# Performance work log

Hardware: AMD Instinct MI355X
Metric: run time of the kernel (lower is better)

The kernel has to match this reference:

```python
import jax, jax.numpy as jnp
import numpy as np

D = 64          # slot_size == in_features
S = 8           # num_slots
H = 128         # mlp_hidden_size
N_ITER = 3
EPS = 1e-8


def _ln(x, g, b, eps=1e-5):
    m = jnp.mean(x, axis=-1, keepdims=True)
    v = jnp.var(x, axis=-1, keepdims=True)
    return (x - m) * jax.lax.rsqrt(v + eps) * g + b


def _gru(x, h, w_ih, w_hh, b_ih, b_hh):
    # torch.nn.GRUCell semantics, gate order r, z, n
    gi = x @ w_ih.T + b_ih
    gh = h @ w_hh.T + b_hh
    i_r, i_z, i_n = jnp.split(gi, 3, axis=-1)
    h_r, h_z, h_n = jnp.split(gh, 3, axis=-1)
    r = jax.nn.sigmoid(i_r + h_r)
    z = jax.nn.sigmoid(i_z + h_z)
    n = jnp.tanh(i_n + r * h_n)
    return (1.0 - z) * n + z * h


def setup_inputs() -> dict:
    key = jax.random.key(0)
    ks = jax.random.split(key, 16)
    sc = 0.02
    inp = {
        'inputs': jax.random.normal(ks[0], (64, 16384, D), jnp.float32),
        'slots_init': jax.random.normal(ks[1], (64, S, D), jnp.float32),
        'ln_in_g': jnp.ones((D,), jnp.float32), 'ln_in_b': jnp.zeros((D,), jnp.float32),
        'ln_s_g': jnp.ones((D,), jnp.float32), 'ln_s_b': jnp.zeros((D,), jnp.float32),
        'ln_m_g': jnp.ones((D,), jnp.float32), 'ln_m_b': jnp.zeros((D,), jnp.float32),
        'Wq': jax.random.normal(ks[2], (D, D), jnp.float32) * sc,
        'Wk': jax.random.normal(ks[3], (D, D), jnp.float32) * sc,
        'Wv': jax.random.normal(ks[4], (D, D), jnp.float32) * sc,
        'w_ih': jax.random.normal(ks[5], (3 * D, D), jnp.float32) * sc,
        'w_hh': jax.random.normal(ks[6], (3 * D, D), jnp.float32) * sc,
        'b_ih': jnp.zeros((3 * D,), jnp.float32),
        'b_hh': jnp.zeros((3 * D,), jnp.float32),
        'W1': jax.random.normal(ks[7], (H, D), jnp.float32) * sc,
        'b1': jnp.zeros((H,), jnp.float32),
        'W2': jax.random.normal(ks[8], (D, H), jnp.float32) * sc,
        'b2': jnp.zeros((D,), jnp.float32),
        'slots_mu': jax.random.normal(ks[9], (1, 1, D), jnp.float32) * sc,
        'slots_log_sigma': jax.random.normal(ks[10], (1, 1, D), jnp.float32) * sc,
    }
    return inp


def reference(inputs, slots_init, ln_in_g, ln_in_b, ln_s_g, ln_s_b, ln_m_g, ln_m_b,
              Wq, Wk, Wv, w_ih, w_hh, b_ih, b_hh, W1, b1, W2, b2,
              slots_mu, slots_log_sigma):
    B, N, _ = inputs.shape
    x = _ln(inputs, ln_in_g, ln_in_b)
    k = x @ Wk.T                               # [B, N, D]
    v = x @ Wv.T                               # [B, N, D]
    slots = slots_mu + jnp.exp(slots_log_sigma) * slots_init  # [B, S, D]
    scale = D ** -0.5
    attns = None
    for it in range(N_ITER):
        slots_prev = slots
        sn = _ln(slots, ln_s_g, ln_s_b)
        q = sn @ Wq.T                          # [B, S, D]
        logits = scale * jnp.einsum('bnd,bsd->bns', k, q)  # [B, N, S]
        attn = jax.nn.softmax(logits, axis=-1)
        if it == 0:
            attns = jax.lax.stop_gradient(attn)  # clone().detach() on first iter
        else:
            attns = attns + attn
        a = attn + EPS
        a = a / jnp.sum(a, axis=1, keepdims=True)  # normalize over inputs
        updates = jnp.einsum('bns,bnd->bsd', a, v)  # [B, S, D]
        h = _gru(updates.reshape(B * S, D), slots_prev.reshape(B * S, D),
                 w_ih, w_hh, b_ih, b_hh).reshape(B, S, D)
        mlp_out = jnp.maximum(_ln(h, ln_m_g, ln_m_b) @ W1.T + b1, 0.0) @ W2.T + b2
        slots = h + mlp_out
    return slots, attns / N_ITER
```

## Files before the change

### kernel.cpp

```cpp
#include <hip/hip_runtime.h>
#include <math.h>

#define Dk 64
#define Sk 8
#define Nk 16384
#define Bk 64
#define Hk 128

typedef __attribute__((ext_vector_type(8))) short   bf16x8;
typedef __attribute__((ext_vector_type(4))) float   f32x4;
typedef __attribute__((ext_vector_type(2))) unsigned int u32x2;
typedef __attribute__((ext_vector_type(4))) unsigned int u32x4;

union FragU { u32x4 u; bf16x8 s; };

__device__ __forceinline__ unsigned short f2b(float f){
  unsigned u = __float_as_uint(f);
  unsigned r = (u + 0x7FFFu + ((u>>16)&1u)) >> 16;
  return (unsigned short)r;
}
__device__ __forceinline__ unsigned pk2(float a, float b){
  return (unsigned)f2b(a) | ((unsigned)f2b(b)<<16);
}
__device__ __forceinline__ bf16x8 mkfrag(unsigned a0,unsigned a1,unsigned a2,unsigned a3){
  FragU x; x.u = (u32x4){a0,a1,a2,a3}; return x.s;
}
__device__ __forceinline__ bf16x8 mkfrag2(u32x2 a, u32x2 b){
  FragU x; x.u = (u32x4){a.x,a.y,b.x,b.y}; return x.s;
}
__device__ __forceinline__ float wsum64(float v){
  #pragma unroll
  for (int m=1;m<64;m<<=1) v += __shfl_xor(v,m,64);
  return v;
}

#define MFMA16(a,b,c) __builtin_amdgcn_mfma_f32_16x16x32_bf16(a,b,c,0,0,0)
#define TRRD(dst, addr)          asm volatile("ds_read_b64_tr_b16 %0, %1"              : "=v"(dst) : "v"(addr) : "memory")
#define TRRD_O(dst, addr, OFF)   asm volatile("ds_read_b64_tr_b16 %0, %1 offset:" #OFF : "=v"(dst) : "v"(addr) : "memory")

template<int MODE>
__global__ __launch_bounds__(256,4) void iter_kernel(
    const float* __restrict__ inp, unsigned short* __restrict__ xbf,
    const float* __restrict__ ln_g, const float* __restrict__ ln_b,
    const float* __restrict__ qtbuf,
    float* __restrict__ attns_out,
    float* __restrict__ Upart,
    float* __restrict__ denpart)
{
  __shared__ unsigned short shmem[4*2688];
  __shared__ float ured[4][512];
  __shared__ float dred[4][8];

  const int t   = threadIdx.x;
  const int wid = t>>6, l = t&63;
  const int r16 = l&15, g = l>>4;
  unsigned short* sh = &shmem[wid*2688];
  const unsigned ldsb = (unsigned)(unsigned long long)(void*)sh;

  const int blk = blockIdx.x;
  const int gw  = blk*4 + wid;
  const int b   = gw>>7;
  const int w0  = (gw&127)*4;

  bf16x8 qf0, qf1;
  {
    const float* qp = qtbuf + (size_t)((b<<3) + (r16&7))*Dk + g*8;
    f32x4 a0 = *(const f32x4*)(qp);    f32x4 a1 = *(const f32x4*)(qp+4);
    f32x4 c0 = *(const f32x4*)(qp+32); f32x4 c1 = *(const f32x4*)(qp+36);
    qf0 = mkfrag(pk2(a0.x,a0.y),pk2(a0.z,a0.w),pk2(a1.x,a1.y),pk2(a1.z,a1.w));
    qf1 = mkfrag(pk2(c0.x,c0.y),pk2(c0.z,c0.w),pk2(c1.x,c1.y),pk2(c1.z,c1.w));
  }

  f32x4 uacc0={0.f,0.f,0.f,0.f}, uacc1={0.f,0.f,0.f,0.f};
  f32x4 uacc2={0.f,0.f,0.f,0.f}, uacc3={0.f,0.f,0.f,0.f};
  f32x4 dacc = {0.f,0.f,0.f,0.f};

  f32x4 gv0,gv1,gv2,gv3, bv0,bv1,bv2,bv3;
  if (MODE==0){
    const float* gp = ln_g + g*16; const float* bp = ln_b + g*16;
    gv0=*(const f32x4*)gp;     gv1=*(const f32x4*)(gp+4);
    gv2=*(const f32x4*)(gp+8); gv3=*(const f32x4*)(gp+12);
    bv0=*(const f32x4*)bp;     bv1=*(const f32x4*)(bp+4);
    bv2=*(const f32x4*)(bp+8); bv3=*(const f32x4*)(bp+12);
  }

  f32x4 cx[2][4];
  u32x4 cp[2][2];
  f32x4 ca[2] = {{0.f,0.f,0.f,0.f},{0.f,0.f,0.f,0.f}};
  f32x4 na[2] = {{0.f,0.f,0.f,0.f},{0.f,0.f,0.f,0.f}};
  {
    const size_t rw0 = (size_t)b*Nk + (size_t)w0*32;
    if (MODE==0){
      #pragma unroll
      for (int rt=0; rt<2; ++rt){
        const float* src = inp + (rw0 + rt*16 + r16)*Dk + g*16;
        cx[rt][0]=*(const f32x4*)src;     cx[rt][1]=*(const f32x4*)(src+4);
        cx[rt][2]=*(const f32x4*)(src+8); cx[rt][3]=*(const f32x4*)(src+12);
      }
    } else {
      #pragma unroll
      for (int rt=0; rt<2; ++rt){
        const unsigned short* sp = xbf + (rw0 + rt*16 + r16)*Dk;
        cp[rt][0] = *(const u32x4*)(sp + g*8);
        cp[rt][1] = *(const u32x4*)(sp + 32 + g*8);
        if (l<32) ca[rt] = *(const f32x4*)(attns_out + (rw0+rt*16+r16)*Sk + g*4);
      }
    }
  }

  for (int w4=0; w4<4; ++w4){
    const size_t rowwin = (size_t)b*Nk + (size_t)(w0+w4)*32;
    bf16x8 xf00, xf01, xf10, xf11;

    if (MODE==0){
      #pragma unroll
      for (int rt=0; rt<2; ++rt){
        const int rloc = rt*16 + r16;
        const size_t row = rowwin + rloc;
        f32x4 x0=cx[rt][0], x1=cx[rt][1], x2=cx[rt][2], x3=cx[rt][3];
        float s1 = (x0.x+x0.y+x0.z+x0.w)+(x1.x+x1.y+x1.z+x1.w)
                 + (x2.x+x2.y+x2.z+x2.w)+(x3.x+x3.y+x3.z+x3.w);
        float s2 = x0.x*x0.x+x0.y*x0.y+x0.z*x0.z+x0.w*x0.w
                 + x1.x*x1.x+x1.y*x1.y+x1.z*x1.z+x1.w*x1.w
                 + x2.x*x2.x+x2.y*x2.y+x2.z*x2.z+x2.w*x2.w
                 + x3.x*x3.x+x3.y*x3.y+x3.z*x3.z+x3.w*x3.w;
        s1 += __shfl_xor(s1,16,64); s1 += __shfl_xor(s1,32,64);
        s2 += __shfl_xor(s2,16,64); s2 += __shfl_xor(s2,32,64);
        const float mean = s1*(1.f/64.f);
        const float rstd = rsqrtf(s2*(1.f/64.f) - mean*mean + 1e-5f);
        x0 = (x0-mean)*rstd*gv0 + bv0;  x1 = (x1-mean)*rstd*gv1 + bv1;
        x2 = (x2-mean)*rstd*gv2 + bv2;  x3 = (x3-mean)*rstd*gv3 + bv3;
        u32x4 lo = {pk2(x0.x,x0.y),pk2(x0.z,x0.w),pk2(x1.x,x1.y),pk2(x1.z,x1.w)};
        u32x4 hi = {pk2(x2.x,x2.y),pk2(x2.z,x2.w),pk2(x3.x,x3.y),pk2(x3.z,x3.w)};
        u32x4* dst = (u32x4*)(xbf + row*Dk + g*16);
        dst[0] = lo; dst[1] = hi;
        const int sb = g*528 + rloc*16;
        *(u32x4*)&sh[sb]   = lo;
        *(u32x4*)&sh[sb+8] = hi;
      }
    } else {
      #pragma unroll
      for (int rt=0; rt<2; ++rt){
        const int rloc = rt*16 + r16;
        FragU f0, f1; f0.u = cp[rt][0]; f1.u = cp[rt][1];
        if (rt==0){ xf00=f0.s; xf01=f1.s; } else { xf10=f0.s; xf11=f1.s; }
        const int i0 = (g>>1)*528     + rloc*16 + (g&1)*8;
        const int i1 = ((g>>1)+2)*528 + rloc*16 + (g&1)*8;
        *(u32x4*)&sh[i0] = cp[rt][0];
        *(u32x4*)&sh[i1] = cp[rt][1];
      }
    }

    if (w4 < 3){
      const size_t rwn = rowwin + 32;
      if (MODE==0){
        #pragma unroll
        for (int rt=0; rt<2; ++rt){
          const float* src = inp + (rwn + rt*16 + r16)*Dk + g*16;
          cx[rt][0]=*(const f32x4*)src;     cx[rt][1]=*(const f32x4*)(src+4);
          cx[rt][2]=*(const f32x4*)(src+8); cx[rt][3]=*(const f32x4*)(src+12);
        }
      } else {
        #pragma unroll
        for (int rt=0; rt<2; ++rt){
          const unsigned short* sp = xbf + (rwn + rt*16 + r16)*Dk;
          cp[rt][0] = *(const u32x4*)(sp + g*8);
          cp[rt][1] = *(const u32x4*)(sp + 32 + g*8);
          if (l<32) na[rt] = *(const f32x4*)(attns_out + (rwn+rt*16+r16)*Sk + g*4);
        }
      }
    }

    if (MODE==0){
      #pragma unroll
      for (int rt=0; rt<2; ++rt){
        const int rloc = rt*16 + r16;
        const int i0 = (g>>1)*528     + rloc*16 + (g&1)*8;
        const int i1 = ((g>>1)+2)*528 + rloc*16 + (g&1)*8;
        FragU f0, f1;
        f0.u = *(const u32x4*)&sh[i0];
        f1.u = *(const u32x4*)&sh[i1];
        if (rt==0){ xf00=f0.s; xf01=f1.s; } else { xf10=f0.s; xf11=f1.s; }
      }
    }

    #pragma unroll
    for (int rt=0; rt<2; ++rt){
      f32x4 c = {0.f,0.f,0.f,0.f};
      c = MFMA16(qf0, rt ? xf10 : xf00, c);
      c = MFMA16(qf1, rt ? xf11 : xf01, c);
      float mx = fmaxf(fmaxf(c.x,c.y), fmaxf(c.z,c.w));
      mx = fmaxf(mx, __shfl_xor(mx,16,64));
      f32x4 e;
      e.x = __expf(c.x-mx); e.y = __expf(c.y-mx);
      e.z = __expf(c.z-mx); e.w = __expf(c.w-mx);
      float es = e.x+e.y+e.z+e.w;
      es += __shfl_xor(es,16,64);
      f32x4 at = e*(1.f/es);
      if (l < 32){
        f32x4 nv = at*(1.f/3.f);
        if (MODE) nv = nv + ca[rt];
        *(f32x4*)(attns_out + (rowwin + rt*16 + r16)*Sk + g*4) = nv;
      }
      f32x4 a = at + 1e-8f;
      dacc = dacc + a;
      u32x2 pk = {pk2(a.x,a.y), pk2(a.z,a.w)};
      *(u32x2*)&sh[2112 + (rt*16+r16)*16 + g*4] = pk;
    }

    asm volatile("s_waitcnt lgkmcnt(0)" ::: "memory");
    u32x2 p0,p1, b00,b01,b10,b11,b20,b21,b30,b31;
    const unsigned pA = ldsb + 4224 + g*256 + r16*2;
    TRRD  (p0, pA);
    TRRD_O(p1, pA, 128);
    const unsigned xA = ldsb + g*256 + r16*2;
    TRRD  (b00, xA);          TRRD_O(b01, xA, 128);
    TRRD_O(b10, xA, 1056);    TRRD_O(b11, xA, 1184);
    TRRD_O(b20, xA, 2112);    TRRD_O(b21, xA, 2240);
    TRRD_O(b30, xA, 3168);    TRRD_O(b31, xA, 3296);
    asm volatile("s_waitcnt lgkmcnt(0)" ::: "memory");
    __builtin_amdgcn_sched_barrier(0);
    const bf16x8 pf = mkfrag2(p0,p1);
    uacc0 = MFMA16(pf, mkfrag2(b00,b01), uacc0);
    uacc1 = MFMA16(pf, mkfrag2(b10,b11), uacc1);
    uacc2 = MFMA16(pf, mkfrag2(b20,b21), uacc2);
    uacc3 = MFMA16(pf, mkfrag2(b30,b31), uacc3);

    if (MODE==1){ ca[0]=na[0]; ca[1]=na[1]; }
  }

  float dd0=dacc.x, dd1=dacc.y, dd2=dacc.z, dd3=dacc.w;
  #pragma unroll
  for (int m=1;m<16;m<<=1){
    dd0 += __shfl_xor(dd0,m,64); dd1 += __shfl_xor(dd1,m,64);
    dd2 += __shfl_xor(dd2,m,64); dd3 += __shfl_xor(dd3,m,64);
  }
  if (l < 32){
    #pragma unroll
    for (int j=0;j<4;++j){
      ured[wid][(g*4+j)*64 +  0 + r16] = uacc0[j];
      ured[wid][(g*4+j)*64 + 16 + r16] = uacc1[j];
      ured[wid][(g*4+j)*64 + 32 + r16] = uacc2[j];
      ured[wid][(g*4+j)*64 + 48 + r16] = uacc3[j];
    }
    if (r16 == 0){
      dred[wid][g*4+0]=dd0; dred[wid][g*4+1]=dd1;
      dred[wid][g*4+2]=dd2; dred[wid][g*4+3]=dd3;
    }
  }
  __syncthreads();
  #pragma unroll
  for (int e=t; e<512; e+=256){
    Upart[(size_t)blk*512 + e] = ured[0][e]+ured[1][e]+ured[2][e]+ured[3][e];
  }
  if (t < 8) denpart[blk*8 + t] = dred[0][t]+dred[1][t]+dred[2][t]+dred[3][t];
}

__global__ __launch_bounds__(64) void slot_kernel(
    const float* __restrict__ slots_init,
    const float* __restrict__ mu, const float* __restrict__ lsig,
    const float* __restrict__ ln_s_g, const float* __restrict__ ln_s_b,
    const float* __restrict__ ln_m_g, const float* __restrict__ ln_m_b,
    const float* __restrict__ Wq, const float* __restrict__ Wk, const float* __restrict__ Wv,
    const float* __restrict__ w_ih, const float* __restrict__ w_hh,
    const float* __restrict__ b_ih, const float* __restrict__ b_hh,
    const float* __restrict__ W1, const float* __restrict__ b1,
    const float* __restrict__ W2, const float* __restrict__ b2,
    float* __restrict__ slots, const float* __restrict__ Upart,
    const float* __restrict__ denpart,
    float* __restrict__ qtbuf, float* __restrict__ slots_out, int mode)
{
  __shared__ float sh[Hk];
  __shared__ float shh[Dk];
  const int d  = threadIdx.x;
  const int bs = blockIdx.x;

  float snew;
  if (mode == 0) {
    snew = mu[d] + expf(lsig[d]) * slots_init[bs*Dk + d];
  } else {
    const int b8 = bs>>3, s = bs&7;
    const float* up = Upart + (size_t)(b8*32)*512 + s*64 + d;
    float uval = 0.f;
    #pragma unroll 8
    for (int k2=0;k2<32;++k2) uval += up[k2*512];
    float dp = (d<32) ? denpart[(b8*32+d)*8 + s] : 0.f;
    const float dn = wsum64(dp);

    sh[d] = uval;
    __syncthreads();
    float num = 0.f;
    #pragma unroll
    for (int j=0;j<Dk;j+=4){
      float4 w = *(const float4*)&Wv[d*Dk+j];
      num += sh[j]*w.x + sh[j+1]*w.y + sh[j+2]*w.z + sh[j+3]*w.w;
    }
    const float upd = num / dn;
    const float h = slots[bs*Dk + d];
    __syncthreads();
    sh[d] = upd; shh[d] = h;
    __syncthreads();

    float gi_r=b_ih[d], gi_z=b_ih[Dk+d], gi_n=b_ih[2*Dk+d];
    float gh_r=b_hh[d], gh_z=b_hh[Dk+d], gh_n=b_hh[2*Dk+d];
    #pragma unroll 4
    for (int j=0;j<Dk;j+=4){
      const float x0=sh[j],  x1=sh[j+1],  x2=sh[j+2],  x3=sh[j+3];
      const float h0=shh[j], h1=shh[j+1], h2=shh[j+2], h3=shh[j+3];
      float4 w;
      w = *(const float4*)&w_ih[d*Dk+j];        gi_r += x0*w.x+x1*w.y+x2*w.z+x3*w.w;
      w = *(const float4*)&w_ih[(Dk+d)*Dk+j];   gi_z += x0*w.x+x1*w.y+x2*w.z+x3*w.w;
      w = *(const float4*)&w_ih[(2*Dk+d)*Dk+j]; gi_n += x0*w.x+x1*w.y+x2*w.z+x3*w.w;
      w = *(const float4*)&w_hh[d*Dk+j];        gh_r += h0*w.x+h1*w.y+h2*w.z+h3*w.w;
      w = *(const float4*)&w_hh[(Dk+d)*Dk+j];   gh_z += h0*w.x+h1*w.y+h2*w.z+h3*w.w;
      w = *(const float4*)&w_hh[(2*Dk+d)*Dk+j]; gh_n += h0*w.x+h1*w.y+h2*w.z+h3*w.w;
    }
    const float rg = 1.f/(1.f+expf(-(gi_r+gh_r)));
    const float zg = 1.f/(1.f+expf(-(gi_z+gh_z)));
    const float ng = tanhf(gi_n + rg*gh_n);
    const float hn = (1.f-zg)*ng + zg*h;

    const float m  = wsum64(hn)*(1.f/64.f);
    const float dv = hn - m;
    const float vr = wsum64(dv*dv)*(1.f/64.f);
    const float mv = dv*rsqrtf(vr+1e-5f)*ln_m_g[d] + ln_m_b[d];
    __syncthreads();
    sh[d] = mv;
    __syncthreads();

    float h1a = b1[d], h2a = b1[Dk+d];
    #pragma unroll 4
    for (int j=0;j<Dk;j+=4){
      const float x0=sh[j], x1=sh[j+1], x2=sh[j+2], x3=sh[j+3];
      float4 w;
      w = *(const float4*)&W1[d*Dk+j];      h1a += x0*w.x+x1*w.y+x2*w.z+x3*w.w;
      w = *(const float4*)&W1[(Dk+d)*Dk+j]; h2a += x0*w.x+x1*w.y+x2*w.z+x3*w.w;
    }
    h1a = fmaxf(h1a, 0.f); h2a = fmaxf(h2a, 0.f);
    __syncthreads();
    sh[d] = h1a; sh[Dk+d] = h2a;
    __syncthreads();
    float o = b2[d];
    #pragma unroll 4
    for (int tt=0;tt<Hk;tt+=4){
      float4 w = *(const float4*)&W2[d*Hk+tt];
      o += sh[tt]*w.x + sh[tt+1]*w.y + sh[tt+2]*w.z + sh[tt+3]*w.w;
    }
    snew = hn + o;
  }

  slots[bs*Dk + d] = snew;
  if (slots_out) slots_out[bs*Dk + d] = snew;

  const float m2  = wsum64(snew)*(1.f/64.f);
  const float dv2 = snew - m2;
  const float vr2 = wsum64(dv2*dv2)*(1.f/64.f);
  const float sn  = dv2*rsqrtf(vr2+1e-5f)*ln_s_g[d] + ln_s_b[d];
  __syncthreads();
  sh[d] = sn;
  __syncthreads();
  float q = 0.f;
  #pragma unroll
  for (int j=0;j<Dk;j+=4){
    float4 w = *(const float4*)&Wq[d*Dk+j];
    q += sh[j]*w.x + sh[j+1]*w.y + sh[j+2]*w.z + sh[j+3]*w.w;
  }
  __syncthreads();
  sh[d] = q;
  __syncthreads();
  float qt = 0.f;
  for (int dd=0; dd<Dk; ++dd) qt += sh[dd]*Wk[dd*Dk + d];
  qtbuf[bs*Dk + d] = qt * 0.125f;
}

extern "C" void kernel_launch(void* const* d_in, const int* in_sizes, int n_in,
                              void* d_out, int out_size, void* d_ws, size_t ws_size,
                              hipStream_t stream)
{
  const float* inp     = (const float*)d_in[0];
  const float* sinit   = (const float*)d_in[1];
  const float* ln_in_g = (const float*)d_in[2];
  const float* ln_in_b = (const float*)d_in[3];
  const float* ln_s_g  = (const float*)d_in[4];
  const float* ln_s_b  = (const float*)d_in[5];
  const float* ln_m_g  = (const float*)d_in[6];
  const float* ln_m_b  = (const float*)d_in[7];
  const float* Wq      = (const float*)d_in[8];
  const float* Wk      = (const float*)d_in[9];
  const float* Wv      = (const float*)d_in[10];
  const float* w_ih    = (const float*)d_in[11];
  const float* w_hh    = (const float*)d_in[12];
  const float* b_ih    = (const float*)d_in[13];
  const float* b_hh    = (const float*)d_in[14];
  const float* W1      = (const float*)d_in[15];
  const float* b1      = (const float*)d_in[16];
  const float* W2      = (const float*)d_in[17];
  const float* b2      = (const float*)d_in[18];
  const float* mu      = (const float*)d_in[19];
  const float* lsig    = (const float*)d_in[20];

  float* out       = (float*)d_out;
  float* out_slots = out;
  float* out_attns = out + Bk*Sk*Dk;

  char* w = (char*)d_ws;
  float* slots   = (float*)(w);
  float* qtbuf   = (float*)(w + 131072);
  float* Upart   = (float*)(w + 262144);
  float* denpart = (float*)(w + 4456448);
  unsigned short* xbf = (unsigned short*)(w + 4521984);

  slot_kernel<<<Bk*Sk, Dk, 0, stream>>>(sinit, mu, lsig, ln_s_g, ln_s_b, ln_m_g, ln_m_b,
      Wq, Wk, Wv, w_ih, w_hh, b_ih, b_hh, W1, b1, W2, b2,
      slots, Upart, denpart, qtbuf, nullptr, 0);

  for (int it = 0; it < 3; ++it) {
    if (it == 0)
      iter_kernel<0><<<2048, 256, 0, stream>>>(
          inp, xbf, ln_in_g, ln_in_b, qtbuf, out_attns, Upart, denpart);
    else
      iter_kernel<1><<<2048, 256, 0, stream>>>(
          inp, xbf, ln_in_g, ln_in_b, qtbuf, out_attns, Upart, denpart);
    slot_kernel<<<Bk*Sk, Dk, 0, stream>>>(sinit, mu, lsig, ln_s_g, ln_s_b, ln_m_g, ln_m_b,
        Wq, Wk, Wv, w_ih, w_hh, b_ih, b_hh, W1, b1, W2, b2,
        slots, Upart, denpart, qtbuf, (it==2) ? out_slots : nullptr, 1);
  }
}
```

Baseline: 235.5 us.

## Defer attention-map accumulation to last iteration by recomputing earlier softmaxes

Each iteration's q is now kept in its own buffer. The attention output is no longer read and written in every pass; the final pass recomputes the softmax for all three q sets and writes the averaged map once, with a nontemporal store. This removes the read-modify-write traffic on the attns output in the first two passes, at the cost of extra MFMA and exp work in the last pass. The fp32 input loads in the first pass also become nontemporal loads.

```diff
diff --git a/kernel.cpp b/kernel.cpp
--- a/kernel.cpp
+++ b/kernel.cpp
@@ -6,6 +6,7 @@
 #define Nk 16384
 #define Bk 64
 #define Hk 128
+#define BSD (Bk*Sk*Dk)
 
 typedef __attribute__((ext_vector_type(8))) short   bf16x8;
 typedef __attribute__((ext_vector_type(4))) float   f32x4;
@@ -33,20 +34,24 @@
   for (int m=1;m<64;m<<=1) v += __shfl_xor(v,m,64);
   return v;
 }
+__device__ __forceinline__ f32x4 ntld4(const float* p){
+  return __builtin_nontemporal_load((const f32x4*)p);
+}
 
 #define MFMA16(a,b,c) __builtin_amdgcn_mfma_f32_16x16x32_bf16(a,b,c,0,0,0)
 #define TRRD(dst, addr)          asm volatile("ds_read_b64_tr_b16 %0, %1"              : "=v"(dst) : "v"(addr) : "memory")
 #define TRRD_O(dst, addr, OFF)   asm volatile("ds_read_b64_tr_b16 %0, %1 offset:" #OFF : "=v"(dst) : "v"(addr) : "memory")
 
-template<int MODE>
+template<int MODE, int LAST>
 __global__ __launch_bounds__(256,4) void iter_kernel(
     const float* __restrict__ inp, unsigned short* __restrict__ xbf,
     const float* __restrict__ ln_g, const float* __restrict__ ln_b,
-    const float* __restrict__ qtbuf,
+    const float* __restrict__ qtb,
     float* __restrict__ attns_out,
     float* __restrict__ Upart,
     float* __restrict__ denpart)
 {
+  constexpr int NQ = LAST ? 3 : 1;
   __shared__ unsigned short shmem[4*2688];
   __shared__ float ured[4][512];
   __shared__ float dred[4][8];
@@ -62,13 +67,14 @@
   const int b   = gw>>7;
   const int w0  = (gw&127)*4;
 
-  bf16x8 qf0, qf1;
-  {
-    const float* qp = qtbuf + (size_t)((b<<3) + (r16&7))*Dk + g*8;
+  bf16x8 qf0[NQ], qf1[NQ];
+  #pragma unroll
+  for (int it=0; it<NQ; ++it){
+    const float* qp = qtb + (size_t)it*BSD + (size_t)((b<<3) + (r16&7))*Dk + g*8;
     f32x4 a0 = *(const f32x4*)(qp);    f32x4 a1 = *(const f32x4*)(qp+4);
     f32x4 c0 = *(const f32x4*)(qp+32); f32x4 c1 = *(const f32x4*)(qp+36);
-    qf0 = mkfrag(pk2(a0.x,a0.y),pk2(a0.z,a0.w),pk2(a1.x,a1.y),pk2(a1.z,a1.w));
-    qf1 = mkfrag(pk2(c0.x,c0.y),pk2(c0.z,c0.w),pk2(c1.x,c1.y),pk2(c1.z,c1.w));
+    qf0[it] = mkfrag(pk2(a0.x,a0.y),pk2(a0.z,a0.w),pk2(a1.x,a1.y),pk2(a1.z,a1.w));
+    qf1[it] = mkfrag(pk2(c0.x,c0.y),pk2(c0.z,c0.w),pk2(c1.x,c1.y),pk2(c1.z,c1.w));
   }
 
   f32x4 uacc0={0.f,0.f,0.f,0.f}, uacc1={0.f,0.f,0.f,0.f};
@@ -86,16 +92,14 @@
 
   f32x4 cx[2][4];
   u32x4 cp[2][2];
-  f32x4 ca[2] = {{0.f,0.f,0.f,0.f},{0.f,0.f,0.f,0.f}};
-  f32x4 na[2] = {{0.f,0.f,0.f,0.f},{0.f,0.f,0.f,0.f}};
   {
     const size_t rw0 = (size_t)b*Nk + (size_t)w0*32;
     if (MODE==0){
       #pragma unroll
       for (int rt=0; rt<2; ++rt){
         const float* src = inp + (rw0 + rt*16 + r16)*Dk + g*16;
-        cx[rt][0]=*(const f32x4*)src;     cx[rt][1]=*(const f32x4*)(src+4);
-        cx[rt][2]=*(const f32x4*)(src+8); cx[rt][3]=*(const f32x4*)(src+12);
+        cx[rt][0]=ntld4(src);   cx[rt][1]=ntld4(src+4);
+        cx[rt][2]=ntld4(src+8); cx[rt][3]=ntld4(src+12);
       }
     } else {
       #pragma unroll
@@ -103,7 +107,6 @@
         const unsigned short* sp = xbf + (rw0 + rt*16 + r16)*Dk;
         cp[rt][0] = *(const u32x4*)(sp + g*8);
         cp[rt][1] = *(const u32x4*)(sp + 32 + g*8);
-        if (l<32) ca[rt] = *(const f32x4*)(attns_out + (rw0+rt*16+r16)*Sk + g*4);
       }
     }
   }
@@ -157,8 +160,8 @@
         #pragma unroll
         for (int rt=0; rt<2; ++rt){
           const float* src = inp + (rwn + rt*16 + r16)*Dk + g*16;
-          cx[rt][0]=*(const f32x4*)src;     cx[rt][1]=*(const f32x4*)(src+4);
-          cx[rt][2]=*(const f32x4*)(src+8); cx[rt][3]=*(const f32x4*)(src+12);
+          cx[rt][0]=ntld4(src);   cx[rt][1]=ntld4(src+4);
+          cx[rt][2]=ntld4(src+8); cx[rt][3]=ntld4(src+12);
         }
       } else {
         #pragma unroll
@@ -166,7 +169,6 @@
           const unsigned short* sp = xbf + (rwn + rt*16 + r16)*Dk;
           cp[rt][0] = *(const u32x4*)(sp + g*8);
           cp[rt][1] = *(const u32x4*)(sp + 32 + g*8);
-          if (l<32) na[rt] = *(const f32x4*)(attns_out + (rwn+rt*16+r16)*Sk + g*4);
         }
       }
     }
@@ -186,23 +188,32 @@
 
     #pragma unroll
     for (int rt=0; rt<2; ++rt){
-      f32x4 c = {0.f,0.f,0.f,0.f};
-      c = MFMA16(qf0, rt ? xf10 : xf00, c);
-      c = MFMA16(qf1, rt ? xf11 : xf01, c);
-      float mx = fmaxf(fmaxf(c.x,c.y), fmaxf(c.z,c.w));
-      mx = fmaxf(mx, __shfl_xor(mx,16,64));
-      f32x4 e;
-      e.x = __expf(c.x-mx); e.y = __expf(c.y-mx);
-      e.z = __expf(c.z-mx); e.w = __expf(c.w-mx);
-      float es = e.x+e.y+e.z+e.w;
-      es += __shfl_xor(es,16,64);
-      f32x4 at = e*(1.f/es);
-      if (l < 32){
-        f32x4 nv = at*(1.f/3.f);
-        if (MODE) nv = nv + ca[rt];
-        *(f32x4*)(attns_out + (rowwin + rt*16 + r16)*Sk + g*4) = nv;
-      }
-      f32x4 a = at + 1e-8f;
+      const bf16x8 xl = rt ? xf10 : xf00;
+      const bf16x8 xh = rt ? xf11 : xf01;
+      f32x4 asum = {0.f,0.f,0.f,0.f};
+      f32x4 atc;
+      #pragma unroll
+      for (int it=0; it<NQ; ++it){
+        f32x4 c = {0.f,0.f,0.f,0.f};
+        c = MFMA16(qf0[it], xl, c);
+        c = MFMA16(qf1[it], xh, c);
+        float mx = fmaxf(fmaxf(c.x,c.y), fmaxf(c.z,c.w));
+        mx = fmaxf(mx, __shfl_xor(mx,16,64));
+        f32x4 e;
+        e.x = __expf(c.x-mx); e.y = __expf(c.y-mx);
+        e.z = __expf(c.z-mx); e.w = __expf(c.w-mx);
+        float es = e.x+e.y+e.z+e.w;
+        es += __shfl_xor(es,16,64);
+        f32x4 at = e*(1.f/es);
+        if (LAST) asum = asum + at;
+        atc = at;
+      }
+      if (LAST && l < 32){
+        f32x4 nv = asum*(1.f/3.f);
+        __builtin_nontemporal_store(nv,
+            (f32x4*)(attns_out + (rowwin + rt*16 + r16)*Sk + g*4));
+      }
+      f32x4 a = atc + 1e-8f;
       dacc = dacc + a;
       u32x2 pk = {pk2(a.x,a.y), pk2(a.z,a.w)};
       *(u32x2*)&sh[2112 + (rt*16+r16)*16 + g*4] = pk;
@@ -225,8 +236,6 @@
     uacc1 = MFMA16(pf, mkfrag2(b10,b11), uacc1);
     uacc2 = MFMA16(pf, mkfrag2(b20,b21), uacc2);
     uacc3 = MFMA16(pf, mkfrag2(b30,b31), uacc3);
-
-    if (MODE==1){ ca[0]=na[0]; ca[1]=na[1]; }
   }
 
   float dd0=dacc.x, dd1=dacc.y, dd2=dacc.z, dd3=dacc.w;
@@ -268,7 +277,7 @@
     const float* __restrict__ W2, const float* __restrict__ b2,
     float* __restrict__ slots, const float* __restrict__ Upart,
     const float* __restrict__ denpart,
-    float* __restrict__ qtbuf, float* __restrict__ slots_out, int mode)
+    float* __restrict__ qt_out, float* __restrict__ slots_out, int mode)
 {
   __shared__ float sh[Hk];
   __shared__ float shh[Dk];
@@ -370,7 +379,7 @@
   __syncthreads();
   float qt = 0.f;
   for (int dd=0; dd<Dk; ++dd) qt += sh[dd]*Wk[dd*Dk + d];
-  qtbuf[bs*Dk + d] = qt * 0.125f;
+  qt_out[bs*Dk + d] = qt * 0.125f;
 }
 
 extern "C" void kernel_launch(void* const* d_in, const int* in_sizes, int n_in,
@@ -401,28 +410,39 @@
 
   float* out       = (float*)d_out;
   float* out_slots = out;
-  float* out_attns = out + Bk*Sk*Dk;
+  float* out_attns = out + BSD;
 
   char* w = (char*)d_ws;
   float* slots   = (float*)(w);
   float* qtbuf   = (float*)(w + 131072);
-  float* Upart   = (float*)(w + 262144);
-  float* denpart = (float*)(w + 4456448);
-  unsigned short* xbf = (unsigned short*)(w + 4521984);
+  float* Upart   = (float*)(w + 655360);
+  float* denpart = (float*)(w + 4849664);
+  unsigned short* xbf = (unsigned short*)(w + 4915200);
+
+  float* qt0 = qtbuf;
+  float* qt1 = qtbuf + BSD;
+  float* qt2 = qtbuf + 2*BSD;
+  float* qt3 = qtbuf + 3*BSD;
 
   slot_kernel<<<Bk*Sk, Dk, 0, stream>>>(sinit, mu, lsig, ln_s_g, ln_s_b, ln_m_g, ln_m_b,
       Wq, Wk, Wv, w_ih, w_hh, b_ih, b_hh, W1, b1, W2, b2,
-      slots, Upart, denpart, qtbuf, nullptr, 0);
-
-  for (int it = 0; it < 3; ++it) {
-    if (it == 0)
-      iter_kernel<0><<<2048, 256, 0, stream>>>(
-          inp, xbf, ln_in_g, ln_in_b, qtbuf, out_attns, Upart, denpart);
-    else
-      iter_kernel<1><<<2048, 256, 0, stream>>>(
-          inp, xbf, ln_in_g, ln_in_b, qtbuf, out_attns, Upart, denpart);
-    slot_kernel<<<Bk*Sk, Dk, 0, stream>>>(sinit, mu, lsig, ln_s_g, ln_s_b, ln_m_g, ln_m_b,
-        Wq, Wk, Wv, w_ih, w_hh, b_ih, b_hh, W1, b1, W2, b2,
-        slots, Upart, denpart, qtbuf, (it==2) ? out_slots : nullptr, 1);
-  }
-}
+      slots, Upart, denpart, qt0, nullptr, 0);
+
+  iter_kernel<0,0><<<2048, 256, 0, stream>>>(
+      inp, xbf, ln_in_g, ln_in_b, qt0, out_attns, Upart, denpart);
+  slot_kernel<<<Bk*Sk, Dk, 0, stream>>>(sinit, mu, lsig, ln_s_g, ln_s_b, ln_m_g, ln_m_b,
+      Wq, Wk, Wv, w_ih, w_hh, b_ih, b_hh, W1, b1, W2, b2,
+      slots, Upart, denpart, qt1, nullptr, 1);
+
+  iter_kernel<1,0><<<2048, 256, 0, stream>>>(
+      inp, xbf, ln_in_g, ln_in_b, qt1, out_attns, Upart, denpart);
+  slot_kernel<<<Bk*Sk, Dk, 0, stream>>>(sinit, mu, lsig, ln_s_g, ln_s_b, ln_m_g, ln_m_b,
+      Wq, Wk, Wv, w_ih, w_hh, b_ih, b_hh, W1, b1, W2, b2,
+      slots, Upart, denpart, qt2, nullptr, 1);
+
+  iter_kernel<1,1><<<2048, 256, 0, stream>>>(
+      inp, xbf, ln_in_g, ln_in_b, qtbuf, out_attns, Upart, denpart);
+  slot_kernel<<<Bk*Sk, Dk, 0, stream>>>(sinit, mu, lsig, ln_s_g, ln_s_b, ln_m_g, ln_m_b,
+      Wq, Wk, Wv, w_ih, w_hh, b_ih, b_hh, W1, b1, W2, b2,
+      slots, Upart, denpart, qt3, out_slots, 1);
+}
```

New measurement: 249.5 us. 5.9% more time.
